# Performance work log

Measured on AMD Instinct MI355X. Metric: run time of the kernel, lower is better.

Reference implementation:

```python
import jax, jax.numpy as jnp
import numpy as np
from jax import lax

B, T, D_BERT, H_LSTM, L = 32, 512, 768, 256, 9


def setup_inputs() -> dict:
    key = jax.random.key(0)
    ks = jax.random.split(key, 10)
    def rn(k, shape, s=0.02):
        return jax.random.normal(k, shape, dtype=jnp.float32) * s
    return {
        "seq_out": jax.random.normal(ks[0], (B, T, D_BERT), dtype=jnp.float32),
        "attention_mask": jnp.ones((B, T), dtype=jnp.int32),
        "labels": jax.random.randint(ks[1], (B, T), 0, L),
        "w_ih_f": rn(ks[2], (4 * H_LSTM, D_BERT)),
        "w_hh_f": rn(ks[3], (4 * H_LSTM, H_LSTM)),
        "b_f": jnp.zeros((4 * H_LSTM,), jnp.float32),
        "w_ih_b": rn(ks[4], (4 * H_LSTM, D_BERT)),
        "w_hh_b": rn(ks[5], (4 * H_LSTM, H_LSTM)),
        "b_b": jnp.zeros((4 * H_LSTM,), jnp.float32),
        "w_tag": rn(ks[6], (L, 2 * H_LSTM)),
        "b_tag": jnp.zeros((L,), jnp.float32),
        "start_trans": rn(ks[7], (L,), 0.1),
        "end_trans": rn(ks[8], (L,), 0.1),
        "trans": rn(ks[9], (L, L), 0.1),
    }


def _lstm_dir(x, w_ih, w_hh, b):
    # x: [T, B, D]; torch gate order: i, f, g, o
    Bb, H = x.shape[1], w_hh.shape[1]
    def step(carry, x_t):
        h, c = carry
        g = x_t @ w_ih.T + h @ w_hh.T + b
        i, f, gg, o = jnp.split(g, 4, axis=-1)
        c = jax.nn.sigmoid(f) * c + jax.nn.sigmoid(i) * jnp.tanh(gg)
        h = jax.nn.sigmoid(o) * jnp.tanh(c)
        return (h, c), h
    init = (jnp.zeros((Bb, H), x.dtype), jnp.zeros((Bb, H), x.dtype))
    _, hs = lax.scan(step, init, x)
    return hs  # [T, B, H]


def _emissions(seq_out, w_ih_f, w_hh_f, b_f, w_ih_b, w_hh_b, b_b, w_tag, b_tag):
    x = seq_out.transpose(1, 0, 2)  # [T, B, D]
    hf = _lstm_dir(x, w_ih_f, w_hh_f, b_f)
    hb = _lstm_dir(x[::-1], w_ih_b, w_hh_b, b_b)[::-1]
    h = jnp.concatenate([hf, hb], axis=-1)  # [T, B, 2H] (dropout: eval mode, identity)
    return (h @ w_tag.T + b_tag).transpose(1, 0, 2).astype(jnp.float32)  # [B, T, L]


def _crf_llh(em, tags, mask, start, end, trans):
    # numerator: score of the gold path
    em_sc = jnp.take_along_axis(em, tags[..., None], axis=2)[..., 0]  # [B, T]
    tr_sc = trans[tags[:, :-1], tags[:, 1:]]  # [B, T-1]
    num = start[tags[:, 0]] + em_sc[:, 0] + jnp.sum((tr_sc + em_sc[:, 1:]) * mask[:, 1:], axis=1)
    last_idx = (jnp.sum(mask, axis=1) - 1).astype(jnp.int32)
    last_tags = jnp.take_along_axis(tags, last_idx[:, None], axis=1)[:, 0]
    num = num + end[last_tags]
    # denominator: log-partition via forward algorithm (sequential logsumexp scan)
    def step(score, inp):
        em_t, m_t = inp
        nxt = jax.nn.logsumexp(score[:, :, None] + trans[None] + em_t[:, None, :], axis=1)
        return jnp.where(m_t[:, None] > 0, nxt, score), None
    score0 = start + em[:, 0]
    score, _ = lax.scan(step, score0, (em[:, 1:].transpose(1, 0, 2), mask[:, 1:].T))
    denom = jax.nn.logsumexp(score + end, axis=1)
    return num - denom


def _crf_decode(em, mask, start, end, trans):
    Ll = em.shape[2]
    def step(score, inp):
        em_t, m_t = inp
        comb = score[:, :, None] + trans[None]  # [B, prev, cur]
        nxt = jnp.max(comb, axis=1) + em_t
        bp = jnp.argmax(comb, axis=1)  # [B, L]
        keep = m_t[:, None] > 0
        return jnp.where(keep, nxt, score), jnp.where(keep, bp, jnp.arange(Ll)[None, :])
    score0 = start + em[:, 0]
    final, bps = lax.scan(step, score0, (em[:, 1:].transpose(1, 0, 2), mask[:, 1:].T))
    last = jnp.argmax(final + end, axis=1)  # [B]
    def back(tag, bp_t):
        prev = jnp.take_along_axis(bp_t, tag[:, None], axis=1)[:, 0]
        return prev, prev
    _, earlier = lax.scan(back, last, bps, reverse=True)  # [T-1, B]
    return jnp.concatenate([earlier, last[None]], axis=0).T  # [B, T]


def reference(seq_out, attention_mask, labels, w_ih_f, w_hh_f, b_f, w_ih_b, w_hh_b, b_b, w_tag, b_tag, start_trans, end_trans, trans):
    em = _emissions(seq_out, w_ih_f, w_hh_f, b_f, w_ih_b, w_hh_b, b_b, w_tag, b_tag)
    mask = attention_mask.astype(jnp.float32)
    lbl = jnp.where(labels == -100, 0, labels)
    loss = -jnp.mean(_crf_llh(em, lbl, mask, start_trans, end_trans, trans))
    preds = _crf_decode(em, attention_mask, start_trans, end_trans, trans)
    return em, loss, preds
```

## Files before the change

### kernel.cpp

```cpp
#include <hip/hip_runtime.h>
#include <cmath>


#define NB 32
#define NT 512
#define ND 768
#define NH 256
#define NG 1024
#define NC 2048
#define NL 9
#define NHC 512
#define PPD 32
#define HPAD 260
#define GPAD 40
#define NBUF (2 * NB * NH)

static const size_t OFF_WIHT  = 0;
static const size_t OFF_WHHT  = 1572864;
static const size_t OFF_XPART = 2097152;
static const size_t OFF_HCAT  = 35651584;
static const size_t OFF_HG    = 44040192;
static const size_t OFF_CTR   = 44072960;

__global__ void prep(const float* __restrict__ wihf, const float* __restrict__ wihb,
                     const float* __restrict__ whhf, const float* __restrict__ whhb,
                     float* __restrict__ w_ihT, float* __restrict__ w_hhT,
                     float* __restrict__ d_loss, int* __restrict__ flags) {
  int idx = blockIdx.x * 256 + threadIdx.x;
  if (idx == 0) d_loss[0] = 0.f;
  if (idx < 1024) flags[idx] = 0;
  if (idx < 1572864) {
    int k = idx >> 11;
    int c = idx & 2047;
    int d = c >> 10;
    int j = c & 1023;
    w_ihT[idx] = d ? wihb[j * ND + k] : wihf[j * ND + k];
  } else {
    int i2 = idx - 1572864;
    int d = i2 >> 18;
    int r = i2 & 262143;
    int k = r >> 10;
    int j = r & 1023;
    w_hhT[i2] = d ? whhb[j * NH + k] : whhf[j * NH + k];
  }
}

__global__ __launch_bounds__(256, 2)
void gemm_x(const float* __restrict__ x, const float* __restrict__ wT,
            const float* __restrict__ bf, const float* __restrict__ bb,
            float* __restrict__ xpart) {
  __shared__ float As[8][128];
  __shared__ float Bs[8][128];
  const int tid = threadIdx.x;
  const int tx = tid & 15, ty = tid >> 4;
  const int r0 = blockIdx.y * 128, c0 = blockIdx.x * 128;

  float acc[8][8] = {};

  const int arow = tid >> 1;
  const int akq  = (tid & 1) * 4;
  const int rA = r0 + arow;
  const float* aptr = x + ((size_t)((rA & 31) * NT + (rA >> 5)) * ND) + akq;
  const int bk = tid >> 5;
  const int bc = (tid & 31) * 4;
  const float* bptr = wT + (size_t)bk * NC + c0 + bc;

  for (int k0 = 0; k0 < ND; k0 += 8) {
    float4 av = *(const float4*)(aptr + k0);
    float4 bv = *(const float4*)(bptr + (size_t)k0 * NC);
    __syncthreads();
    As[akq + 0][arow] = av.x;
    As[akq + 1][arow] = av.y;
    As[akq + 2][arow] = av.z;
    As[akq + 3][arow] = av.w;
    *(float4*)&Bs[bk][bc] = bv;
    __syncthreads();
#pragma unroll
    for (int k = 0; k < 8; ++k) {
      float4 a0 = *(const float4*)&As[k][ty * 8];
      float4 a1 = *(const float4*)&As[k][ty * 8 + 4];
      float4 b0 = *(const float4*)&Bs[k][tx * 8];
      float4 b1 = *(const float4*)&Bs[k][tx * 8 + 4];
      float am[8] = {a0.x, a0.y, a0.z, a0.w, a1.x, a1.y, a1.z, a1.w};
      float bm[8] = {b0.x, b0.y, b0.z, b0.w, b1.x, b1.y, b1.z, b1.w};
#pragma unroll
      for (int i = 0; i < 8; ++i)
#pragma unroll
        for (int j = 0; j < 8; ++j) acc[i][j] += am[i] * bm[j];
    }
  }

  const int cbase = c0 + tx * 8;
  float bias[8];
#pragma unroll
  for (int j = 0; j < 8; ++j) {
    int c = cbase + j;
    bias[j] = (c < NG) ? bf[c] : bb[c - NG];
  }
#pragma unroll
  for (int i = 0; i < 8; ++i) {
    int r = r0 + ty * 8 + i;
    float4 v0 = {acc[i][0] + bias[0], acc[i][1] + bias[1],
                 acc[i][2] + bias[2], acc[i][3] + bias[3]};
    float4 v1 = {acc[i][4] + bias[4], acc[i][5] + bias[5],
                 acc[i][6] + bias[6], acc[i][7] + bias[7]};
    *(float4*)(xpart + (size_t)r * NC + cbase) = v0;
    *(float4*)(xpart + (size_t)r * NC + cbase + 4) = v1;
  }
}

__global__ __launch_bounds__(256, 1)
void lstm_scan(const float* __restrict__ whhT, const float* __restrict__ xpart,
               float* __restrict__ hcat, float* __restrict__ hG,
               int* __restrict__ flags) {
  __shared__ float wS[256 * 32];
  __shared__ float hS[32 * HPAD];
  __shared__ float gS[32 * GPAD];
  const int tid = threadIdx.x;
  const int d = blockIdx.x >> 5;
  const int m = blockIdx.x & 31;

  const float* wsrc = whhT + (size_t)d * NH * NG;
  for (int it = 0; it < 32; ++it) {
    int i = it * 256 + tid;
    int k = i >> 5, l = i & 31;
    int g = l >> 3, u2 = l & 7;
    wS[k * 32 + l] = wsrc[(size_t)k * NG + g * 256 + m * 8 + u2];
  }
  for (int i = tid; i < 32 * HPAD; i += 256) hS[i] = 0.f;
  __syncthreads();

  const int b = tid >> 3;
  const int cg = tid & 7;
  const int u = tid & 7;
  const int l0 = cg * 4;
  const int g4 = l0 >> 3, u04 = l0 & 7;
  const int col4 = g4 * 256 + m * 8 + u04;
  int* flagd = flags + d * PPD;
  const int lane = tid & 63;

  float c = 0.f;
  for (int s = 0; s < NT; ++s) {
    const int t = d ? (NT - 1 - s) : s;
    float4 xv = *(const float4*)(xpart + ((size_t)(t * NB + b) * NC) + d * NG + col4);
    float4 acc = {0.f, 0.f, 0.f, 0.f};
    const float* hrow = &hS[b * HPAD];
    for (int k0 = 0; k0 < NH; k0 += 4) {
      float4 hv = *(const float4*)(hrow + k0);
      {
        float4 wv = *(const float4*)(&wS[(k0 + 0) * 32 + l0]);
        acc.x += hv.x * wv.x; acc.y += hv.x * wv.y; acc.z += hv.x * wv.z; acc.w += hv.x * wv.w;
      }
      {
        float4 wv = *(const float4*)(&wS[(k0 + 1) * 32 + l0]);
        acc.x += hv.y * wv.x; acc.y += hv.y * wv.y; acc.z += hv.y * wv.z; acc.w += hv.y * wv.w;
      }
      {
        float4 wv = *(const float4*)(&wS[(k0 + 2) * 32 + l0]);
        acc.x += hv.z * wv.x; acc.y += hv.z * wv.y; acc.z += hv.z * wv.z; acc.w += hv.z * wv.w;
      }
      {
        float4 wv = *(const float4*)(&wS[(k0 + 3) * 32 + l0]);
        acc.x += hv.w * wv.x; acc.y += hv.w * wv.y; acc.z += hv.w * wv.z; acc.w += hv.w * wv.w;
      }
    }
    acc.x += xv.x; acc.y += xv.y; acc.z += xv.z; acc.w += xv.w;
    *(float4*)(&gS[b * GPAD + l0]) = acc;
    __syncthreads();

    float gi = gS[b * GPAD + u];
    float gf = gS[b * GPAD + 8 + u];
    float gg = gS[b * GPAD + 16 + u];
    float go = gS[b * GPAD + 24 + u];
    float ii = 1.f / (1.f + expf(-gi));
    float ff = 1.f / (1.f + expf(-gf));
    float tg = tanhf(gg);
    float oo = 1.f / (1.f + expf(-go));
    c = ff * c + ii * tg;
    float h = oo * tanhf(c);
    hcat[((size_t)(b * NT + t)) * NHC + d * NH + m * 8 + u] = h;

    if (s < NT - 1) {
      float* dst = hG + ((s & 1) ? NBUF : 0) + d * 8192 + m * 256;
      __hip_atomic_store(&dst[tid], h, __ATOMIC_RELAXED, __HIP_MEMORY_SCOPE_AGENT);
      __syncthreads();
      if (tid == 0)
        __hip_atomic_store(&flagd[m], s + 1, __ATOMIC_RELEASE,
                           __HIP_MEMORY_SCOPE_AGENT);
      {
        long long t0 = wall_clock64();
        for (;;) {
          int v = (lane < PPD)
              ? __hip_atomic_load(&flagd[lane], __ATOMIC_RELAXED,
                                  __HIP_MEMORY_SCOPE_AGENT)
              : 0x7fffffff;
          if (__ballot(v > s) == ~0ULL) break;
          if (wall_clock64() - t0 > 5000000LL) break;
        }
      }
      __syncthreads();
      const unsigned long long* src = (const unsigned long long*)
          (hG + ((s & 1) ? NBUF : 0) + d * 8192);
#pragma unroll
      for (int i = 0; i < 16; ++i) {
        int f = i * 256 + tid;
        unsigned long long v = __hip_atomic_load(&src[f], __ATOMIC_RELAXED,
                                                 __HIP_MEMORY_SCOPE_AGENT);
        union { unsigned long long uu; float ff2[2]; } cv;
        cv.uu = v;
        int mq = f >> 7;
        int r = f & 127;
        int bb = r >> 2;
        int u2 = (r & 3) * 2;
        hS[bb * HPAD + mq * 8 + u2] = cv.ff2[0];
        hS[bb * HPAD + mq * 8 + u2 + 1] = cv.ff2[1];
      }
      __syncthreads();
    }
  }
}

__global__ void emissions(const float* __restrict__ hcat, const float* __restrict__ wtag,
                          const float* __restrict__ btag, float* __restrict__ em) {
  __shared__ float wS[NL * NHC];
  const int tid = threadIdx.x;
  for (int i = tid; i < NL * NHC; i += 256) wS[i] = wtag[i];
  __syncthreads();
  const int w = tid >> 6, l = tid & 63;
  const int r = blockIdx.x * 4 + w;
  const float* hp = hcat + (size_t)r * NHC;
  float acc[NL] = {};
#pragma unroll
  for (int rep = 0; rep < 8; ++rep) {
    float hv = hp[l + rep * 64];
#pragma unroll
    for (int j = 0; j < NL; ++j) acc[j] += hv * wS[j * NHC + l + rep * 64];
  }
#pragma unroll
  for (int j = 0; j < NL; ++j) {
#pragma unroll
    for (int off = 32; off; off >>= 1) acc[j] += __shfl_xor(acc[j], off, 64);
  }
  if (l == 0) {
#pragma unroll
    for (int j = 0; j < NL; ++j) em[(size_t)r * NL + j] = acc[j] + btag[j];
  }
}

__global__ void crf_fwd(const float* __restrict__ em, const int* __restrict__ mask,
                        const int* __restrict__ labels, const float* __restrict__ start,
                        const float* __restrict__ endt, const float* __restrict__ trans,
                        float* __restrict__ d_loss) {
  __shared__ float emS[NT * NL];
  __shared__ float maskS[NT];
  __shared__ int lblS[NT];
  const int b = blockIdx.x;
  const int tid = threadIdx.x;
  for (int i = tid; i < NT * NL; i += 64) emS[i] = em[(size_t)b * NT * NL + i];
  for (int i = tid; i < NT; i += 64) {
    maskS[i] = (float)mask[b * NT + i];
    int lb = labels[b * NT + i];
    lblS[i] = (lb == -100) ? 0 : lb;
  }
  __syncthreads();

  float part = 0.f, msum = 0.f;
  for (int t = tid; t < NT; t += 64) {
    msum += maskS[t];
    if (t >= 1)
      part += (trans[lblS[t - 1] * NL + lblS[t]] + emS[t * NL + lblS[t]]) * maskS[t];
  }
#pragma unroll
  for (int off = 32; off; off >>= 1) {
    part += __shfl_xor(part, off, 64);
    msum += __shfl_xor(msum, off, 64);
  }

  const int j = tid >> 2, q = tid & 3;
  const bool leader = (q == 0) && (j < NL);
  float tr0 = 0.f, tr1 = 0.f, tr2 = -1e30f;
  float score = 0.f;
  if (tid < 36) {
    tr0 = trans[q * NL + j];
    tr1 = trans[(q + 4) * NL + j];
    if (q == 0) tr2 = trans[8 * NL + j];
    if (leader) score = start[j] + emS[j];
  }
  for (int t = 1; t < NT; ++t) {
    float s0 = __shfl(score, q * 4, 64);
    float s1 = __shfl(score, (q + 4) * 4, 64);
    float s2 = __shfl(score, 32, 64);
    float v0 = s0 + tr0, v1 = s1 + tr1;
    float v2 = (q == 0) ? (s2 + tr2) : -1e30f;
    float m = fmaxf(fmaxf(v0, v1), v2);
    m = fmaxf(m, __shfl_xor(m, 1, 4));
    m = fmaxf(m, __shfl_xor(m, 2, 4));
    float e = expf(v0 - m) + expf(v1 - m) + ((q == 0) ? expf(v2 - m) : 0.f);
    e += __shfl_xor(e, 1, 4);
    e += __shfl_xor(e, 2, 4);
    if (leader) {
      float nxt = m + logf(e) + emS[t * NL + j];
      score = (maskS[t] > 0.f) ? nxt : score;
    }
  }
  float vs[NL];
  float mx = -1e30f;
#pragma unroll
  for (int jj = 0; jj < NL; ++jj) {
    float sj = __shfl(score, jj * 4, 64) + endt[jj];
    vs[jj] = sj;
    mx = fmaxf(mx, sj);
  }
  float se = 0.f;
#pragma unroll
  for (int jj = 0; jj < NL; ++jj) se += expf(vs[jj] - mx);
  float denom = mx + logf(se);
  if (tid == 0) {
    int li = (int)(msum - 0.5f);
    float num = start[lblS[0]] + emS[lblS[0]] + part + endt[lblS[li]];
    atomicAdd(d_loss, -(num - denom) * (1.f / 32.f));
  }
}

__global__ void crf_viterbi(const float* __restrict__ em, const int* __restrict__ mask,
                            const float* __restrict__ start, const float* __restrict__ endt,
                            const float* __restrict__ trans, float* __restrict__ preds) {
  __shared__ float emS[NT * NL];
  __shared__ int maskS[NT];
  __shared__ short bpS[(NT - 1) * NL];
  __shared__ short tagS[NT];
  const int b = blockIdx.x;
  const int tid = threadIdx.x;
  for (int i = tid; i < NT * NL; i += 64) emS[i] = em[(size_t)b * NT * NL + i];
  for (int i = tid; i < NT; i += 64) maskS[i] = mask[b * NT + i];
  __syncthreads();

  const int j = tid >> 2, q = tid & 3;
  const bool leader = (q == 0) && (j < NL);
  float tr0 = 0.f, tr1 = 0.f, tr2 = -1e30f;
  float score = 0.f;
  if (tid < 36) {
    tr0 = trans[q * NL + j];
    tr1 = trans[(q + 4) * NL + j];
    if (q == 0) tr2 = trans[8 * NL + j];
    if (leader) score = start[j] + emS[j];
  }
  for (int t = 1; t < NT; ++t) {
    float s0 = __shfl(score, q * 4, 64);
    float s1 = __shfl(score, (q + 4) * 4, 64);
    float s2 = __shfl(score, 32, 64);
    float v0 = s0 + tr0, v1 = s1 + tr1;
    float v2 = (q == 0) ? (s2 + tr2) : -1e30f;
    float bv = v0;
    int bi = q;
    if (v1 > bv) { bv = v1; bi = q + 4; }
    if (q == 0 && v2 > bv) { bv = v2; bi = 8; }
#pragma unroll
    for (int off = 1; off <= 2; off <<= 1) {
      float ov = __shfl_xor(bv, off, 4);
      int oi = __shfl_xor(bi, off, 4);
      if (ov > bv || (ov == bv && oi < bi)) { bv = ov; bi = oi; }
    }
    if (leader) {
      int keep = maskS[t];
      float nxt = bv + emS[t * NL + j];
      bpS[(t - 1) * NL + j] = keep ? (short)bi : (short)j;
      score = keep ? nxt : score;
    }
  }
  float fv[NL];
#pragma unroll
  for (int jj = 0; jj < NL; ++jj) fv[jj] = __shfl(score, jj * 4, 64) + endt[jj];
  if (tid == 0) {
    int last = 0;
    float bvv = fv[0];
#pragma unroll
    for (int jj = 1; jj < NL; ++jj)
      if (fv[jj] > bvv) { bvv = fv[jj]; last = jj; }
    tagS[NT - 1] = (short)last;
    for (int t = NT - 1; t >= 1; --t) tagS[t - 1] = bpS[(t - 1) * NL + tagS[t]];
  }
  __syncthreads();
  for (int i = tid; i < NT; i += 64) preds[(size_t)b * NT + i] = (float)tagS[i];
}

extern "C" void kernel_launch(void* const* d_in, const int* in_sizes, int n_in,
                              void* d_out, int out_size, void* d_ws, size_t ws_size,
                              hipStream_t stream) {
  const float* seq_out = (const float*)d_in[0];
  const int* attn = (const int*)d_in[1];
  const int* labels = (const int*)d_in[2];
  const float* w_ih_f = (const float*)d_in[3];
  const float* w_hh_f = (const float*)d_in[4];
  const float* b_f = (const float*)d_in[5];
  const float* w_ih_b = (const float*)d_in[6];
  const float* w_hh_b = (const float*)d_in[7];
  const float* b_b = (const float*)d_in[8];
  const float* w_tag = (const float*)d_in[9];
  const float* b_tag = (const float*)d_in[10];
  const float* start_t = (const float*)d_in[11];
  const float* end_t = (const float*)d_in[12];
  const float* trans = (const float*)d_in[13];
  (void)in_sizes; (void)n_in; (void)out_size; (void)ws_size;

  float* ws = (float*)d_ws;
  float* w_ihT = ws + OFF_WIHT;
  float* w_hhT = ws + OFF_WHHT;
  float* xpart = ws + OFF_XPART;
  float* hcat = ws + OFF_HCAT;
  float* hG = ws + OFF_HG;
  int* flags = (int*)(ws + OFF_CTR);

  float* em = (float*)d_out;
  float* d_loss = em + NB * NT * NL;
  float* preds = d_loss + 1;

  prep<<<8192, 256, 0, stream>>>(w_ih_f, w_ih_b, w_hh_f, w_hh_b, w_ihT, w_hhT, d_loss, flags);
  gemm_x<<<dim3(16, 128), 256, 0, stream>>>(seq_out, w_ihT, b_f, b_b, xpart);
  lstm_scan<<<64, 256, 0, stream>>>(w_hhT, xpart, hcat, hG, flags);
  emissions<<<4096, 256, 0, stream>>>(hcat, w_tag, b_tag, em);
  crf_fwd<<<32, 64, 0, stream>>>(em, attn, labels, start_t, end_t, trans, d_loss);
  crf_viterbi<<<32, 64, 0, stream>>>(em, attn, start_t, end_t, trans, preds);
}
```

Baseline: 6.418 ms.

## Interleave both LSTM directions in one block with split-K recurrent matvec

The recurrent scan now runs 32 blocks of 512 threads, each handling the same hidden slice for both forward and backward directions, in place of 64 blocks of 256 threads with one direction each. The hidden-to-gate product is split over two K halves with partial sums reduced through shared memory. Each direction publishes its flag as soon as its step is done, so the backward step computes while the forward exchange is still in flight and the wait for one direction overlaps the other's work. The aim is to halve the grid-wide synchronising block count and hide inter-block latency, at the cost of more barriers per step and a much shorter spin timeout.

Result: faster. 5.851 ms (-8.8%).

```diff
diff --git a/kernel.cpp b/kernel.cpp
--- a/kernel.cpp
+++ b/kernel.cpp
@@ -12,8 +12,10 @@
 #define NHC 512
 #define PPD 32
 #define HPAD 260
-#define GPAD 40
+#define HSZ  (32 * HPAD)
 #define NBUF (2 * NB * NH)
+
+typedef float f32x4 __attribute__((ext_vector_type(4)));
 
 static const size_t OFF_WIHT  = 0;
 static const size_t OFF_WHHT  = 1572864;
@@ -109,113 +111,132 @@
   }
 }
 
-__global__ __launch_bounds__(256, 1)
+__global__ __launch_bounds__(512, 1)
 void lstm_scan(const float* __restrict__ whhT, const float* __restrict__ xpart,
                float* __restrict__ hcat, float* __restrict__ hG,
                int* __restrict__ flags) {
-  __shared__ float wS[256 * 32];
-  __shared__ float hS[32 * HPAD];
-  __shared__ float gS[32 * GPAD];
+  __shared__ float wS[2 * 256 * 32];
+  __shared__ float hS[2 * HSZ];
+  __shared__ float pSw[32 * 68];
   const int tid = threadIdx.x;
-  const int d = blockIdx.x >> 5;
-  const int m = blockIdx.x & 31;
-
-  const float* wsrc = whhT + (size_t)d * NH * NG;
-  for (int it = 0; it < 32; ++it) {
-    int i = it * 256 + tid;
-    int k = i >> 5, l = i & 31;
-    int g = l >> 3, u2 = l & 7;
-    wS[k * 32 + l] = wsrc[(size_t)k * NG + g * 256 + m * 8 + u2];
-  }
-  for (int i = tid; i < 32 * HPAD; i += 256) hS[i] = 0.f;
+  const int m = blockIdx.x;
+
+  for (int dd = 0; dd < 2; ++dd) {
+    const float* wsrc = whhT + (size_t)dd * NH * NG;
+    for (int it = 0; it < 16; ++it) {
+      int i = it * 512 + tid;
+      int k = i >> 5, l = i & 31;
+      int g = l >> 3, u2 = l & 7;
+      wS[(dd * 256 + k) * 32 + l] = wsrc[(size_t)k * NG + g * 256 + m * 8 + u2];
+    }
+  }
+  for (int i = tid; i < 2 * HSZ; i += 512) hS[i] = 0.f;
   __syncthreads();
 
-  const int b = tid >> 3;
-  const int cg = tid & 7;
-  const int u = tid & 7;
-  const int l0 = cg * 4;
-  const int g4 = l0 >> 3, u04 = l0 & 7;
-  const int col4 = g4 * 256 + m * 8 + u04;
-  int* flagd = flags + d * PPD;
-  const int lane = tid & 63;
-
-  float c = 0.f;
+  const int kh = tid >> 8;
+  const int pr = tid & 255;
+  const int pb = pr >> 3;
+  const int pcg = pr & 7;
+  const int l0 = pcg * 4;
+  const int ub = tid >> 3;
+  const int uu = tid & 7;
+  const int c0i = (uu >> 2) * 8 + (uu & 3);
+
+  float cf = 0.f, cb = 0.f;
+
   for (int s = 0; s < NT; ++s) {
-    const int t = d ? (NT - 1 - s) : s;
-    float4 xv = *(const float4*)(xpart + ((size_t)(t * NB + b) * NC) + d * NG + col4);
-    float4 acc = {0.f, 0.f, 0.f, 0.f};
-    const float* hrow = &hS[b * HPAD];
-    for (int k0 = 0; k0 < NH; k0 += 4) {
-      float4 hv = *(const float4*)(hrow + k0);
-      {
-        float4 wv = *(const float4*)(&wS[(k0 + 0) * 32 + l0]);
-        acc.x += hv.x * wv.x; acc.y += hv.x * wv.y; acc.z += hv.x * wv.z; acc.w += hv.x * wv.w;
+    const int tf = s, tb = NT - 1 - s;
+
+    float xf[4], xb[4];
+    if (tid < 256) {
+      const float* xpf = xpart + ((size_t)(tf * NB + ub) * NC) + m * 8 + uu;
+      const float* xpb = xpart + ((size_t)(tb * NB + ub) * NC) + NG + m * 8 + uu;
+#pragma unroll
+      for (int g = 0; g < 4; ++g) { xf[g] = xpf[g * 256]; xb[g] = xpb[g * 256]; }
+    }
+
+    for (int d = 0; d < 2; ++d) {
+      const float* hrow = hS + d * HSZ + pb * HPAD + kh * 128;
+      const float* wcol = wS + (size_t)(d * 256 + kh * 128) * 32 + l0;
+      f32x4 acc = {0.f, 0.f, 0.f, 0.f};
+#pragma unroll 4
+      for (int kk = 0; kk < 128; kk += 4) {
+        f32x4 hv = *(const f32x4*)(hrow + kk);
+        f32x4 w0 = *(const f32x4*)(wcol + (size_t)(kk + 0) * 32);
+        f32x4 w1 = *(const f32x4*)(wcol + (size_t)(kk + 1) * 32);
+        f32x4 w2 = *(const f32x4*)(wcol + (size_t)(kk + 2) * 32);
+        f32x4 w3 = *(const f32x4*)(wcol + (size_t)(kk + 3) * 32);
+        acc += hv.x * w0;
+        acc += hv.y * w1;
+        acc += hv.z * w2;
+        acc += hv.w * w3;
       }
-      {
-        float4 wv = *(const float4*)(&wS[(k0 + 1) * 32 + l0]);
-        acc.x += hv.y * wv.x; acc.y += hv.y * wv.y; acc.z += hv.y * wv.z; acc.w += hv.y * wv.w;
+      *(f32x4*)(pSw + pb * 68 + (pcg * 2 + kh) * 4) = acc;
+      __syncthreads();
+
+      if (tid < 256) {
+        const float* pS = pSw + ub * 68;
+        const float* xv = d ? xb : xf;
+        float g0 = pS[c0i]      + pS[c0i + 4]  + xv[0];
+        float g1 = pS[c0i + 16] + pS[c0i + 20] + xv[1];
+        float g2 = pS[c0i + 32] + pS[c0i + 36] + xv[2];
+        float g3 = pS[c0i + 48] + pS[c0i + 52] + xv[3];
+        float ii = 1.f / (1.f + expf(-g0));
+        float ff = 1.f / (1.f + expf(-g1));
+        float tg = tanhf(g2);
+        float oo = 1.f / (1.f + expf(-g3));
+        float& cc = d ? cb : cf;
+        cc = ff * cc + ii * tg;
+        float h = oo * tanhf(cc);
+        const int t = d ? tb : tf;
+        hcat[((size_t)(ub * NT + t)) * NHC + d * NH + m * 8 + uu] = h;
+        float* dst = hG + ((s & 1) ? NBUF : 0) + d * 8192 + m * 256 + ub * 8 + uu;
+        __hip_atomic_store(dst, h, __ATOMIC_RELAXED, __HIP_MEMORY_SCOPE_AGENT);
       }
-      {
-        float4 wv = *(const float4*)(&wS[(k0 + 2) * 32 + l0]);
-        acc.x += hv.z * wv.x; acc.y += hv.z * wv.y; acc.z += hv.z * wv.z; acc.w += hv.z * wv.w;
-      }
-      {
-        float4 wv = *(const float4*)(&wS[(k0 + 3) * 32 + l0]);
-        acc.x += hv.w * wv.x; acc.y += hv.w * wv.y; acc.z += hv.w * wv.z; acc.w += hv.w * wv.w;
-      }
-    }
-    acc.x += xv.x; acc.y += xv.y; acc.z += xv.z; acc.w += xv.w;
-    *(float4*)(&gS[b * GPAD + l0]) = acc;
-    __syncthreads();
-
-    float gi = gS[b * GPAD + u];
-    float gf = gS[b * GPAD + 8 + u];
-    float gg = gS[b * GPAD + 16 + u];
-    float go = gS[b * GPAD + 24 + u];
-    float ii = 1.f / (1.f + expf(-gi));
-    float ff = 1.f / (1.f + expf(-gf));
-    float tg = tanhf(gg);
-    float oo = 1.f / (1.f + expf(-go));
-    c = ff * c + ii * tg;
-    float h = oo * tanhf(c);
-    hcat[((size_t)(b * NT + t)) * NHC + d * NH + m * 8 + u] = h;
-
-    if (s < NT - 1) {
-      float* dst = hG + ((s & 1) ? NBUF : 0) + d * 8192 + m * 256;
-      __hip_atomic_store(&dst[tid], h, __ATOMIC_RELAXED, __HIP_MEMORY_SCOPE_AGENT);
       __syncthreads();
       if (tid == 0)
-        __hip_atomic_store(&flagd[m], s + 1, __ATOMIC_RELEASE,
+        __hip_atomic_store(&flags[d * 32 + m], s + 1, __ATOMIC_RELEASE,
                            __HIP_MEMORY_SCOPE_AGENT);
-      {
-        long long t0 = wall_clock64();
-        for (;;) {
-          int v = (lane < PPD)
-              ? __hip_atomic_load(&flagd[lane], __ATOMIC_RELAXED,
-                                  __HIP_MEMORY_SCOPE_AGENT)
-              : 0x7fffffff;
-          if (__ballot(v > s) == ~0ULL) break;
-          if (wall_clock64() - t0 > 5000000LL) break;
+    }
+
+    if (s < NT - 1) {
+      const float* bufpar = hG + ((s & 1) ? NBUF : 0);
+      for (int d = 0; d < 2; ++d) {
+        if (tid < 64) {
+          int* fl = flags + d * 32;
+          long long t0 = wall_clock64();
+          for (;;) {
+            int v = (tid < 32)
+                ? __hip_atomic_load(&fl[tid], __ATOMIC_RELAXED,
+                                    __HIP_MEMORY_SCOPE_AGENT)
+                : 0x7fffffff;
+            if (__ballot(v > s) == ~0ULL) break;
+            if (wall_clock64() - t0 > 200000LL) break;
+          }
         }
+        __syncthreads();
+        const unsigned long long* src = (const unsigned long long*)
+            (bufpar + d * 8192);
+        unsigned long long vv[8];
+#pragma unroll
+        for (int i = 0; i < 8; ++i)
+          vv[i] = __hip_atomic_load(&src[i * 512 + tid], __ATOMIC_RELAXED,
+                                    __HIP_MEMORY_SCOPE_AGENT);
+        float* hd = hS + d * HSZ;
+#pragma unroll
+        for (int i = 0; i < 8; ++i) {
+          int f = i * 512 + tid;
+          union { unsigned long long uu; float ff2[2]; } cv;
+          cv.uu = vv[i];
+          int mq = f >> 7;
+          int r = f & 127;
+          int bb = r >> 2;
+          int u2 = (r & 3) * 2;
+          hd[bb * HPAD + mq * 8 + u2] = cv.ff2[0];
+          hd[bb * HPAD + mq * 8 + u2 + 1] = cv.ff2[1];
+        }
+        if (d == 0) __syncthreads();
       }
-      __syncthreads();
-      const unsigned long long* src = (const unsigned long long*)
-          (hG + ((s & 1) ? NBUF : 0) + d * 8192);
-#pragma unroll
-      for (int i = 0; i < 16; ++i) {
-        int f = i * 256 + tid;
-        unsigned long long v = __hip_atomic_load(&src[f], __ATOMIC_RELAXED,
-                                                 __HIP_MEMORY_SCOPE_AGENT);
-        union { unsigned long long uu; float ff2[2]; } cv;
-        cv.uu = v;
-        int mq = f >> 7;
-        int r = f & 127;
-        int bb = r >> 2;
-        int u2 = (r & 3) * 2;
-        hS[bb * HPAD + mq * 8 + u2] = cv.ff2[0];
-        hS[bb * HPAD + mq * 8 + u2 + 1] = cv.ff2[1];
-      }
-      __syncthreads();
     }
   }
 }
@@ -417,7 +438,7 @@
 
   prep<<<8192, 256, 0, stream>>>(w_ih_f, w_ih_b, w_hh_f, w_hh_b, w_ihT, w_hhT, d_loss, flags);
   gemm_x<<<dim3(16, 128), 256, 0, stream>>>(seq_out, w_ihT, b_f, b_b, xpart);
-  lstm_scan<<<64, 256, 0, stream>>>(w_hhT, xpart, hcat, hG, flags);
+  lstm_scan<<<32, 512, 0, stream>>>(w_hhT, xpart, hcat, hG, flags);
   emissions<<<4096, 256, 0, stream>>>(hcat, w_tag, b_tag, em);
   crf_fwd<<<32, 64, 0, stream>>>(em, attn, labels, start_t, end_t, trans, d_loss);
   crf_viterbi<<<32, 64, 0, stream>>>(em, attn, start_t, end_t, trans, preds);
```
